# Kernel optimization log

Hardware: AMD Instinct MI355X
Metric: run time of the kernel (lower is better)

Reference implementation:

```python
import jax, jax.numpy as jnp
import numpy as np

B, T, C = 2, 2048, 1024
N_HEAD, N_GROUP = 16, 4
N_KV = N_HEAD // N_GROUP          # 4
HEAD_DIM = C // N_HEAD            # 64
ROPE_BASE = 10000.0
INIT_STD = 0.02


def setup_inputs() -> dict:
    key = jax.random.key(0)
    ks = jax.random.split(key, 5)
    kvC = N_KV * HEAD_DIM
    return {
        "x": jax.random.normal(ks[0], (B, T, C), jnp.float32),
        "w_q": jax.random.normal(ks[1], (C, C), jnp.float32) * INIT_STD,
        "b_q": jnp.zeros((C,), jnp.float32),
        "w_k": jax.random.normal(ks[2], (C, kvC), jnp.float32) * INIT_STD,
        "b_k": jnp.zeros((kvC,), jnp.float32),
        "w_v": jax.random.normal(ks[3], (C, kvC), jnp.float32) * INIT_STD,
        "b_v": jnp.zeros((kvC,), jnp.float32),
        "w_o": jax.random.normal(ks[4], (C, C), jnp.float32) * INIT_STD,
        "b_o": jnp.zeros((C,), jnp.float32),
    }


def reference(x, w_q, b_q, w_k, b_k, w_v, b_v, w_o, b_o):
    Bx, Tx, Cx = x.shape
    # projections (torch Linear math with weights stored as [in, out])
    q = (x @ w_q + b_q).reshape(Bx, Tx, N_HEAD, HEAD_DIM).transpose(0, 2, 1, 3)  # [B,H,T,hd]
    k = (x @ w_k + b_k).reshape(Bx, Tx, N_KV, HEAD_DIM).transpose(0, 2, 1, 3)    # [B,KV,T,hd]
    v = (x @ w_v + b_v).reshape(Bx, Tx, N_KV, HEAD_DIM).transpose(0, 2, 1, 3)

    # RoPE with INTERLEAVED pair convention: pairs are (dim 2i, dim 2i+1)
    inv_freq = 1.0 / (ROPE_BASE ** (jnp.arange(0, HEAD_DIM, 2, dtype=jnp.float32) / HEAD_DIM))
    freqs = jnp.arange(Tx, dtype=jnp.float32)[:, None] * inv_freq[None, :]       # [T, hd/2]
    cos, sin = jnp.cos(freqs), jnp.sin(freqs)

    def rope(t):
        tp = t.reshape(*t.shape[:-1], HEAD_DIM // 2, 2)
        e, o = tp[..., 0], tp[..., 1]          # even/odd lanes, [B,h,T,hd/2]
        er = e * cos - o * sin
        orr = e * sin + o * cos
        return jnp.stack([er, orr], axis=-1).reshape(t.shape)

    q, k = rope(q), rope(k)

    # GQA: duplicate each KV head n_group times (consecutively, like repeat_interleave)
    k = jnp.repeat(k, N_GROUP, axis=1)   # [B,H,T,hd]
    v = jnp.repeat(v, N_GROUP, axis=1)

    attn = jnp.einsum('bhqd,bhkd->bhqk', q, k) / np.sqrt(HEAD_DIM).astype(np.float32)
    causal = jnp.tril(jnp.ones((Tx, Tx), bool))
    attn = jnp.where(causal, attn, -jnp.inf)
    attn = jax.nn.softmax(attn, axis=-1)

    out = jnp.einsum('bhqk,bhkd->bhqd', attn, v)            # [B,H,T,hd]
    out = out.transpose(0, 2, 1, 3).reshape(Bx, Tx, Cx)
    return out @ w_o + b_o
```

## Files before the change

### kernel.cpp

```cpp
#include <hip/hip_runtime.h>
#include <hip/hip_bf16.h>

typedef __hip_bfloat16 bf16;
typedef __attribute__((ext_vector_type(8))) short short8_t;
typedef __attribute__((ext_vector_type(4))) short short4_t;
typedef __attribute__((ext_vector_type(4))) float f32x4;

#define B_SZ   2
#define T_SEQ  2048
#define C_DIM  1024
#define NH     16
#define NKV    4
#define HD     64
#define QKVW   1536
#define MTOK   (B_SZ * T_SEQ)

#define LOG2_BASE_OVER_32 0.4152410118609203f
#define Q_SCALE 0.1803368801111204f

__device__ __forceinline__ short f2bs(float f) {
    unsigned u = __float_as_uint(f);
    u += 0x7FFFu + ((u >> 16) & 1u);
    return (short)(u >> 16);
}
__device__ __forceinline__ short f2bs_trunc(float f) {
    return (short)(__float_as_uint(f) >> 16);
}
__device__ __forceinline__ float bs2f(short s) {
    unsigned u = ((unsigned)(unsigned short)s) << 16;
    return __uint_as_float(u);
}
__device__ __forceinline__ float dpp_xor1(float x) {
    return __int_as_float(
        __builtin_amdgcn_update_dpp(0, __float_as_int(x), 0xB1, 0xF, 0xF, true));
}

__device__ __forceinline__ void transpose_tile(
    const float* __restrict__ W, short* __restrict__ Wt,
    int K, int N, int n0, int k0, int tid)
{
    __shared__ float tile[32][33];
    int tx = tid & 31, ty = tid >> 5;
    #pragma unroll
    for (int i = 0; i < 4; ++i)
        tile[ty + 8 * i][tx] = W[(size_t)(k0 + ty + 8 * i) * N + n0 + tx];
    __syncthreads();
    #pragma unroll
    for (int i = 0; i < 4; ++i)
        Wt[(size_t)(n0 + ty + 8 * i) * K + k0 + tx] = f2bs(tile[tx][ty + 8 * i]);
}

__global__ __launch_bounds__(256) void prep_kernel(
    const float* __restrict__ x,
    const float* __restrict__ w_q, const float* __restrict__ w_k,
    const float* __restrict__ w_v, const float* __restrict__ w_o,
    const float* __restrict__ b_q, const float* __restrict__ b_k,
    const float* __restrict__ b_v,
    short* __restrict__ Xb, short* __restrict__ Wqkv, short* __restrict__ Wto,
    float* __restrict__ Bqkv, float2* __restrict__ Tab)
{
    int blk = blockIdx.x, tid = threadIdx.x;
    if (blk < 4096) {
        int i = blk * 1024 + tid * 4;
        float4 v = *(const float4*)(x + i);
        short4_t o;
        o[0] = f2bs(v.x); o[1] = f2bs(v.y); o[2] = f2bs(v.z); o[3] = f2bs(v.w);
        *(short4_t*)(Xb + i) = o;
    } else if (blk < 5120) {
        int l = blk - 4096;
        transpose_tile(w_q, Wqkv, C_DIM, C_DIM, (l & 31) * 32, (l >> 5) * 32, tid);
    } else if (blk < 5376) {
        int l = blk - 5120;
        transpose_tile(w_k, Wqkv + (size_t)1024 * C_DIM, C_DIM, 256,
                       (l & 7) * 32, (l >> 3) * 32, tid);
    } else if (blk < 5632) {
        int l = blk - 5376;
        transpose_tile(w_v, Wqkv + (size_t)1280 * C_DIM, C_DIM, 256,
                       (l & 7) * 32, (l >> 3) * 32, tid);
    } else if (blk < 6656) {
        int l = blk - 5632;
        transpose_tile(w_o, Wto, C_DIM, C_DIM, (l & 31) * 32, (l >> 5) * 32, tid);
    } else if (blk < 6662) {
        int i = (blk - 6656) * 256 + tid;
        float v;
        if (i < 1024)      v = b_q[i];
        else if (i < 1280) v = b_k[i - 1024];
        else               v = b_v[i - 1280];
        Bqkv[i] = v;
    } else {
        int idx = (blk - 6662) * 256 + tid;
        int t = idx >> 5, i = idx & 31;
        float ang = (float)t * exp2f(-(float)i * LOG2_BASE_OVER_32);
        Tab[idx] = make_float2(cosf(ang), sinf(ang));
    }
}

__global__ __launch_bounds__(256) void gemm_qkv(
    const short* __restrict__ A, const short* __restrict__ Bt,
    const float* __restrict__ bias, const float2* __restrict__ Tab,
    short* __restrict__ QKVb, short* __restrict__ Vt)
{
    __shared__ __align__(16) short smem[15360];
    short (*sA)[128][40] = (short(*)[128][40])smem;
    short (*sB)[64][40]  = (short(*)[64][40])(smem + 10240);

    const int K = C_DIM;
    int m0 = blockIdx.y * 128;
    int n0 = blockIdx.x * 64;
    int tid  = threadIdx.x;
    int w    = tid >> 6, lane = tid & 63;
    int quad = lane >> 4, l16 = lane & 15;
    int wm = w & 1, wn = w >> 1;

    f32x4 acc[4][2] = {};

    short8_t ra[2], rb;
    #pragma unroll
    for (int it = 0; it < 2; ++it) {
        int slot = tid + 256 * it, row = slot >> 2, g = (slot & 3) * 8;
        ra[it] = *(const short8_t*)(A + (size_t)(m0 + row) * K + g);
    }
    {
        int row = tid >> 2, g = (tid & 3) * 8;
        rb = *(const short8_t*)(Bt + (size_t)(n0 + row) * K + g);
    }

    int buf = 0;
    for (int k0 = 0; k0 < K; k0 += 32, buf ^= 1) {
        #pragma unroll
        for (int it = 0; it < 2; ++it) {
            int slot = tid + 256 * it, row = slot >> 2, g = (slot & 3) * 8;
            *(short8_t*)&sA[buf][row][g] = ra[it];
        }
        {
            int row = tid >> 2, g = (tid & 3) * 8;
            *(short8_t*)&sB[buf][row][g] = rb;
        }
        if (k0 + 32 < K) {
            #pragma unroll
            for (int it = 0; it < 2; ++it) {
                int slot = tid + 256 * it, row = slot >> 2, g = (slot & 3) * 8;
                ra[it] = *(const short8_t*)(A + (size_t)(m0 + row) * K + k0 + 32 + g);
            }
            int row = tid >> 2, g = (tid & 3) * 8;
            rb = *(const short8_t*)(Bt + (size_t)(n0 + row) * K + k0 + 32 + g);
        }
        __syncthreads();

        short8_t af[4], bfr[2];
        #pragma unroll
        for (int mt = 0; mt < 4; ++mt)
            af[mt] = *(const short8_t*)&sA[buf][wm * 64 + mt * 16 + l16][quad * 8];
        #pragma unroll
        for (int nt = 0; nt < 2; ++nt)
            bfr[nt] = *(const short8_t*)&sB[buf][wn * 32 + nt * 16 + l16][quad * 8];
        #pragma unroll
        for (int mt = 0; mt < 4; ++mt)
            #pragma unroll
            for (int nt = 0; nt < 2; ++nt)
                acc[mt][nt] = __builtin_amdgcn_mfma_f32_16x16x32_bf16(
                    af[mt], bfr[nt], acc[mt][nt], 0, 0, 0);
    }

    if (n0 < 1280) {
        float scale = (n0 < 1024) ? Q_SCALE : 1.0f;
        float sgn   = (l16 & 1) ? 1.0f : -1.0f;
        #pragma unroll
        for (int nt = 0; nt < 2; ++nt) {
            int col = n0 + wn * 32 + nt * 16 + l16;
            int ip  = (col & 63) >> 1;
            float bv = bias[col];
            #pragma unroll
            for (int mt = 0; mt < 4; ++mt) {
                #pragma unroll
                for (int r = 0; r < 4; ++r) {
                    int row = m0 + wm * 64 + mt * 16 + quad * 4 + r;
                    float v = acc[mt][nt][r] + bv;
                    float po = dpp_xor1(v);
                    float2 cs = Tab[(row & (T_SEQ - 1)) * 32 + ip];
                    float res = (v * cs.x + sgn * po * cs.y) * scale;
                    QKVb[(size_t)row * QKVW + col] = f2bs(res);
                }
            }
        }
    } else {
        __syncthreads();
        short (*sT)[136] = (short(*)[136])smem;
        #pragma unroll
        for (int nt = 0; nt < 2; ++nt) {
            int col_l = wn * 32 + nt * 16 + l16;
            float bv = bias[n0 + col_l];
            #pragma unroll
            for (int mt = 0; mt < 4; ++mt)
                #pragma unroll
                for (int r = 0; r < 4; ++r)
                    sT[col_l][wm * 64 + mt * 16 + quad * 4 + r] =
                        f2bs(acc[mt][nt][r] + bv);
        }
        __syncthreads();
        int d0 = n0 - 1280;
        #pragma unroll
        for (int it = 0; it < 4; ++it) {
            int slot = tid + 256 * it;
            int dl = slot >> 4, seg = (slot & 15) * 8;
            *(short8_t*)(Vt + (size_t)(d0 + dl) * MTOK + m0 + seg) =
                *(const short8_t*)&sT[dl][seg];
        }
    }
}

__global__ __launch_bounds__(256) void gemm_mfma_o(
    const short* __restrict__ A, const short* __restrict__ Bt,
    const float* __restrict__ bias, float* __restrict__ C,
    int M, int N, int K)
{
    __shared__ __align__(16) short smem[15360];
    short (*sA)[128][40] = (short(*)[128][40])smem;
    short (*sB)[64][40]  = (short(*)[64][40])(smem + 10240);

    int m0 = blockIdx.y * 128;
    int n0 = blockIdx.x * 64;
    int tid  = threadIdx.x;
    int w    = tid >> 6, lane = tid & 63;
    int quad = lane >> 4, l16 = lane & 15;
    int wm = w & 1, wn = w >> 1;

    f32x4 acc[4][2] = {};

    short8_t ra[2], rb;
    #pragma unroll
    for (int it = 0; it < 2; ++it) {
        int slot = tid + 256 * it, row = slot >> 2, g = (slot & 3) * 8;
        ra[it] = *(const short8_t*)(A + (size_t)(m0 + row) * K + g);
    }
    {
        int row = tid >> 2, g = (tid & 3) * 8;
        rb = *(const short8_t*)(Bt + (size_t)(n0 + row) * K + g);
    }

    int buf = 0;
    for (int k0 = 0; k0 < K; k0 += 32, buf ^= 1) {
        #pragma unroll
        for (int it = 0; it < 2; ++it) {
            int slot = tid + 256 * it, row = slot >> 2, g = (slot & 3) * 8;
            *(short8_t*)&sA[buf][row][g] = ra[it];
        }
        {
            int row = tid >> 2, g = (tid & 3) * 8;
            *(short8_t*)&sB[buf][row][g] = rb;
        }
        if (k0 + 32 < K) {
            #pragma unroll
            for (int it = 0; it < 2; ++it) {
                int slot = tid + 256 * it, row = slot >> 2, g = (slot & 3) * 8;
                ra[it] = *(const short8_t*)(A + (size_t)(m0 + row) * K + k0 + 32 + g);
            }
            int row = tid >> 2, g = (tid & 3) * 8;
            rb = *(const short8_t*)(Bt + (size_t)(n0 + row) * K + k0 + 32 + g);
        }
        __syncthreads();

        short8_t af[4], bfr[2];
        #pragma unroll
        for (int mt = 0; mt < 4; ++mt)
            af[mt] = *(const short8_t*)&sA[buf][wm * 64 + mt * 16 + l16][quad * 8];
        #pragma unroll
        for (int nt = 0; nt < 2; ++nt)
            bfr[nt] = *(const short8_t*)&sB[buf][wn * 32 + nt * 16 + l16][quad * 8];
        #pragma unroll
        for (int mt = 0; mt < 4; ++mt)
            #pragma unroll
            for (int nt = 0; nt < 2; ++nt)
                acc[mt][nt] = __builtin_amdgcn_mfma_f32_16x16x32_bf16(
                    af[mt], bfr[nt], acc[mt][nt], 0, 0, 0);
    }

    #pragma unroll
    for (int mt = 0; mt < 4; ++mt) {
        #pragma unroll
        for (int nt = 0; nt < 2; ++nt) {
            int col = n0 + wn * 32 + nt * 16 + l16;
            float bv = bias[col];
            #pragma unroll
            for (int r = 0; r < 4; ++r) {
                int row = m0 + wm * 64 + mt * 16 + quad * 4 + r;
                C[(size_t)row * N + col] = acc[mt][nt][r] + bv;
            }
        }
    }
}

__global__ __launch_bounds__(256) void attn_mfma9(
    const short* __restrict__ QKV, const short* __restrict__ Vt,
    short* __restrict__ O)
{
    __shared__ __align__(16) short sK [64][72];
    __shared__ __align__(16) short sVt[64][72];
    __shared__ __align__(16) short sP [4][16][72];

    const int tid  = threadIdx.x;
    const int w    = tid >> 6;
    const int lane = tid & 63;
    const int quad = lane >> 4;
    const int l16  = lane & 15;

    int blk = blockIdx.x;
    int grp = blk & 7;
    int tq  = 127 - (blk >> 3);
    int kvh = grp & 3;
    int b   = grp >> 2;
    int h   = kvh * 4 + w;
    int ct  = tq >> 2;
    int tg  = tq * 16 + l16;

    const short* qptr = QKV + ((size_t)(b * T_SEQ) + tq * 16 + l16) * QKVW + h * HD;
    short8_t qf0 = *(const short8_t*)(qptr + quad * 8);
    short8_t qf1 = *(const short8_t*)(qptr + quad * 8 + 32);

    const short* kbase  = QKV + (size_t)b * T_SEQ * QKVW + 1024 + kvh * HD;
    const short* vtbase = Vt + (size_t)(kvh * HD) * MTOK + b * T_SEQ;

    float m_l = -INFINITY, l_l = 0.f;
    f32x4 oacc[4];
    #pragma unroll
    for (int dt = 0; dt < 4; ++dt) oacc[dt] = (f32x4){0.f, 0.f, 0.f, 0.f};

    const int kkey = tid >> 3, kd = (tid & 7) * 8;
    const int vdim = tid >> 3, vseg = (tid & 7) * 8;

    short8_t kr[2], vr[2];
    #pragma unroll
    for (int it = 0; it < 2; ++it) {
        kr[it] = *(const short8_t*)(kbase + (size_t)(kkey + 32 * it) * QKVW + kd);
        vr[it] = *(const short8_t*)(vtbase + (size_t)(vdim + 32 * it) * MTOK + vseg);
    }

    for (int c = 0; c <= ct; ++c) {
        __syncthreads();
        #pragma unroll
        for (int it = 0; it < 2; ++it) {
            *(short8_t*)&sK [kkey + 32 * it][kd]   = kr[it];
            *(short8_t*)&sVt[vdim + 32 * it][vseg] = vr[it];
        }
        __syncthreads();
        if (c < ct) {
            int jn = (c + 1) * 64;
            #pragma unroll
            for (int it = 0; it < 2; ++it) {
                kr[it] = *(const short8_t*)(kbase + (size_t)(jn + kkey + 32 * it) * QKVW + kd);
                vr[it] = *(const short8_t*)(vtbase + (size_t)(vdim + 32 * it) * MTOK + jn + vseg);
            }
        }

        f32x4 sacc[4];
        #pragma unroll
        for (int kt = 0; kt < 4; ++kt) {
            f32x4 z = {0.f, 0.f, 0.f, 0.f};
            short8_t kf0 = *(const short8_t*)&sK[l16 + 16 * kt][quad * 8];
            short8_t kf1 = *(const short8_t*)&sK[l16 + 16 * kt][quad * 8 + 32];
            z = __builtin_amdgcn_mfma_f32_16x16x32_bf16(kf0, qf0, z, 0, 0, 0);
            z = __builtin_amdgcn_mfma_f32_16x16x32_bf16(kf1, qf1, z, 0, 0, 0);
            sacc[kt] = z;
        }

        if (c == ct) {
            int j0 = c * 64;
            #pragma unroll
            for (int kt = 0; kt < 4; ++kt)
                #pragma unroll
                for (int r = 0; r < 4; ++r)
                    if (j0 + 16 * kt + quad * 4 + r > tg) sacc[kt][r] = -INFINITY;
        }

        float vmax = sacc[0][0];
        #pragma unroll
        for (int kt = 0; kt < 4; ++kt)
            #pragma unroll
            for (int r = 0; r < 4; ++r) vmax = fmaxf(vmax, sacc[kt][r]);
        vmax = fmaxf(vmax, __shfl_xor(vmax, 16));
        vmax = fmaxf(vmax, __shfl_xor(vmax, 32));
        float mnew = fmaxf(m_l, vmax);
        float al = exp2f(m_l - mnew);
        m_l = mnew;

        float psum = 0.f;
        #pragma unroll
        for (int kt = 0; kt < 4; ++kt) {
            short4_t pk;
            #pragma unroll
            for (int r = 0; r < 4; ++r) {
                float p = exp2f(sacc[kt][r] - mnew);
                psum += p;
                pk[r] = f2bs_trunc(p);
            }
            *(short4_t*)&sP[w][l16][16 * kt + 4 * quad] = pk;
        }
        psum += __shfl_xor(psum, 16);
        psum += __shfl_xor(psum, 32);
        l_l = l_l * al + psum;

        if (__any(al < 1.f)) {
            #pragma unroll
            for (int r = 0; r < 4; ++r) {
                float alr = __shfl(al, quad * 4 + r);
                #pragma unroll
                for (int dt = 0; dt < 4; ++dt) oacc[dt][r] *= alr;
            }
        }

        short8_t pf0 = *(const short8_t*)&sP[w][l16][quad * 8];
        short8_t pf1 = *(const short8_t*)&sP[w][l16][quad * 8 + 32];
        #pragma unroll
        for (int dt = 0; dt < 4; ++dt) {
            short8_t vf0 = *(const short8_t*)&sVt[16 * dt + l16][quad * 8];
            short8_t vf1 = *(const short8_t*)&sVt[16 * dt + l16][quad * 8 + 32];
            oacc[dt] = __builtin_amdgcn_mfma_f32_16x16x32_bf16(pf0, vf0, oacc[dt], 0, 0, 0);
            oacc[dt] = __builtin_amdgcn_mfma_f32_16x16x32_bf16(pf1, vf1, oacc[dt], 0, 0, 0);
        }
    }

    #pragma unroll
    for (int r = 0; r < 4; ++r) {
        int m = quad * 4 + r;
        float lr = __shfl(l_l, quad * 4 + r);
        float inv = __builtin_amdgcn_rcpf(lr);
        #pragma unroll
        for (int dt = 0; dt < 4; ++dt)
            O[((size_t)b * T_SEQ + tq * 16 + m) * C_DIM + h * HD + 16 * dt + l16] =
                f2bs(oacc[dt][r] * inv);
    }
}

extern "C" void kernel_launch(void* const* d_in, const int* in_sizes, int n_in,
                              void* d_out, int out_size, void* d_ws, size_t ws_size,
                              hipStream_t stream)
{
    const float* x   = (const float*)d_in[0];
    const float* w_q = (const float*)d_in[1];
    const float* b_q = (const float*)d_in[2];
    const float* w_k = (const float*)d_in[3];
    const float* b_k = (const float*)d_in[4];
    const float* w_v = (const float*)d_in[5];
    const float* b_v = (const float*)d_in[6];
    const float* w_o = (const float*)d_in[7];
    const float* b_o = (const float*)d_in[8];
    float* out = (float*)d_out;

    char* ws = (char*)d_ws;
    short*  Xb   = (short*) (ws);
    short*  Ab   = (short*) (ws + ((size_t)8  << 20));
    short*  QKVb = (short*) (ws + ((size_t)16 << 20));
    short*  Wqkv = (short*) (ws + ((size_t)28 << 20));
    short*  Wto  = (short*) (ws + ((size_t)31 << 20));
    float*  Bqkv = (float*) (ws + ((size_t)33 << 20));
    float2* Tab  = (float2*)(ws + ((size_t)33 << 20) + 8192);
    short*  Vt   = (short*) (ws + ((size_t)34 << 20));

    const int M = MTOK;

    prep_kernel<<<6918, 256, 0, stream>>>(
        x, w_q, w_k, w_v, w_o, b_q, b_k, b_v, Xb, Wqkv, Wto, Bqkv, Tab);

    gemm_qkv<<<dim3(QKVW / 64, M / 128), 256, 0, stream>>>(
        Xb, Wqkv, Bqkv, Tab, QKVb, Vt);

    attn_mfma9<<<B_SZ * NKV * 128, 256, 0, stream>>>(QKVb, Vt, Ab);

    gemm_mfma_o<<<dim3(C_DIM / 64, M / 128), 256, 0, stream>>>(
        Ab, Wto, b_o, out, M, C_DIM, C_DIM);
}
```

Before: 174.9 us.

## Pair causal query tiles per attention block and deepen GEMM K-step to 64

The attention kernel now gives each block two query tiles, p and 127-p, so every block does about the same causal work and each K/V tile loaded into shared memory serves both tiles. The grid is halved to match. Separately, both GEMM kernels stage 64-wide K slices instead of 32, halving the number of loop iterations and barriers. The cost is more shared memory and more registers per thread, which may lower occupancy, and each attention block now carries two sets of accumulators.

```diff
diff --git a/kernel.cpp b/kernel.cpp
--- a/kernel.cpp
+++ b/kernel.cpp
@@ -100,9 +100,9 @@
     const float* __restrict__ bias, const float2* __restrict__ Tab,
     short* __restrict__ QKVb, short* __restrict__ Vt)
 {
-    __shared__ __align__(16) short smem[15360];
-    short (*sA)[128][40] = (short(*)[128][40])smem;
-    short (*sB)[64][40]  = (short(*)[64][40])(smem + 10240);
+    __shared__ __align__(16) short smem[26112];
+    short (*sA)[128][68] = (short(*)[128][68])smem;
+    short (*sB)[64][68]  = (short(*)[64][68])(smem + 17408);
 
     const int K = C_DIM;
     int m0 = blockIdx.y * 128;
@@ -114,52 +114,60 @@
 
     f32x4 acc[4][2] = {};
 
-    short8_t ra[2], rb;
+    short8_t ra[4], rb[2];
+    #pragma unroll
+    for (int it = 0; it < 4; ++it) {
+        int slot = tid + 256 * it, row = slot >> 3, g = (slot & 7) * 8;
+        ra[it] = *(const short8_t*)(A + (size_t)(m0 + row) * K + g);
+    }
     #pragma unroll
     for (int it = 0; it < 2; ++it) {
-        int slot = tid + 256 * it, row = slot >> 2, g = (slot & 3) * 8;
-        ra[it] = *(const short8_t*)(A + (size_t)(m0 + row) * K + g);
-    }
-    {
-        int row = tid >> 2, g = (tid & 3) * 8;
-        rb = *(const short8_t*)(Bt + (size_t)(n0 + row) * K + g);
+        int slot = tid + 256 * it, row = slot >> 3, g = (slot & 7) * 8;
+        rb[it] = *(const short8_t*)(Bt + (size_t)(n0 + row) * K + g);
     }
 
     int buf = 0;
-    for (int k0 = 0; k0 < K; k0 += 32, buf ^= 1) {
+    for (int k0 = 0; k0 < K; k0 += 64, buf ^= 1) {
+        #pragma unroll
+        for (int it = 0; it < 4; ++it) {
+            int slot = tid + 256 * it, row = slot >> 3, g = (slot & 7) * 8;
+            *(short8_t*)&sA[buf][row][g] = ra[it];
+        }
         #pragma unroll
         for (int it = 0; it < 2; ++it) {
-            int slot = tid + 256 * it, row = slot >> 2, g = (slot & 3) * 8;
-            *(short8_t*)&sA[buf][row][g] = ra[it];
-        }
-        {
-            int row = tid >> 2, g = (tid & 3) * 8;
-            *(short8_t*)&sB[buf][row][g] = rb;
-        }
-        if (k0 + 32 < K) {
+            int slot = tid + 256 * it, row = slot >> 3, g = (slot & 7) * 8;
+            *(short8_t*)&sB[buf][row][g] = rb[it];
+        }
+        if (k0 + 64 < K) {
+            #pragma unroll
+            for (int it = 0; it < 4; ++it) {
+                int slot = tid + 256 * it, row = slot >> 3, g = (slot & 7) * 8;
+                ra[it] = *(const short8_t*)(A + (size_t)(m0 + row) * K + k0 + 64 + g);
+            }
             #pragma unroll
             for (int it = 0; it < 2; ++it) {
-                int slot = tid + 256 * it, row = slot >> 2, g = (slot & 3) * 8;
-                ra[it] = *(const short8_t*)(A + (size_t)(m0 + row) * K + k0 + 32 + g);
-            }
-            int row = tid >> 2, g = (tid & 3) * 8;
-            rb = *(const short8_t*)(Bt + (size_t)(n0 + row) * K + k0 + 32 + g);
+                int slot = tid + 256 * it, row = slot >> 3, g = (slot & 7) * 8;
+                rb[it] = *(const short8_t*)(Bt + (size_t)(n0 + row) * K + k0 + 64 + g);
+            }
         }
         __syncthreads();
 
-        short8_t af[4], bfr[2];
-        #pragma unroll
-        for (int mt = 0; mt < 4; ++mt)
-            af[mt] = *(const short8_t*)&sA[buf][wm * 64 + mt * 16 + l16][quad * 8];
-        #pragma unroll
-        for (int nt = 0; nt < 2; ++nt)
-            bfr[nt] = *(const short8_t*)&sB[buf][wn * 32 + nt * 16 + l16][quad * 8];
-        #pragma unroll
-        for (int mt = 0; mt < 4; ++mt)
+        #pragma unroll
+        for (int h = 0; h < 2; ++h) {
+            short8_t af[4], bfr[2];
+            #pragma unroll
+            for (int mt = 0; mt < 4; ++mt)
+                af[mt] = *(const short8_t*)&sA[buf][wm * 64 + mt * 16 + l16][quad * 8 + 32 * h];
             #pragma unroll
             for (int nt = 0; nt < 2; ++nt)
-                acc[mt][nt] = __builtin_amdgcn_mfma_f32_16x16x32_bf16(
-                    af[mt], bfr[nt], acc[mt][nt], 0, 0, 0);
+                bfr[nt] = *(const short8_t*)&sB[buf][wn * 32 + nt * 16 + l16][quad * 8 + 32 * h];
+            #pragma unroll
+            for (int mt = 0; mt < 4; ++mt)
+                #pragma unroll
+                for (int nt = 0; nt < 2; ++nt)
+                    acc[mt][nt] = __builtin_amdgcn_mfma_f32_16x16x32_bf16(
+                        af[mt], bfr[nt], acc[mt][nt], 0, 0, 0);
+        }
     }
 
     if (n0 < 1280) {
@@ -214,9 +222,9 @@
     const float* __restrict__ bias, float* __restrict__ C,
     int M, int N, int K)
 {
-    __shared__ __align__(16) short smem[15360];
-    short (*sA)[128][40] = (short(*)[128][40])smem;
-    short (*sB)[64][40]  = (short(*)[64][40])(smem + 10240);
+    __shared__ __align__(16) short smem[26112];
+    short (*sA)[128][68] = (short(*)[128][68])smem;
+    short (*sB)[64][68]  = (short(*)[64][68])(smem + 17408);
 
     int m0 = blockIdx.y * 128;
     int n0 = blockIdx.x * 64;
@@ -227,52 +235,60 @@
 
     f32x4 acc[4][2] = {};
 
-    short8_t ra[2], rb;
+    short8_t ra[4], rb[2];
+    #pragma unroll
+    for (int it = 0; it < 4; ++it) {
+        int slot = tid + 256 * it, row = slot >> 3, g = (slot & 7) * 8;
+        ra[it] = *(const short8_t*)(A + (size_t)(m0 + row) * K + g);
+    }
     #pragma unroll
     for (int it = 0; it < 2; ++it) {
-        int slot = tid + 256 * it, row = slot >> 2, g = (slot & 3) * 8;
-        ra[it] = *(const short8_t*)(A + (size_t)(m0 + row) * K + g);
-    }
-    {
-        int row = tid >> 2, g = (tid & 3) * 8;
-        rb = *(const short8_t*)(Bt + (size_t)(n0 + row) * K + g);
+        int slot = tid + 256 * it, row = slot >> 3, g = (slot & 7) * 8;
+        rb[it] = *(const short8_t*)(Bt + (size_t)(n0 + row) * K + g);
     }
 
     int buf = 0;
-    for (int k0 = 0; k0 < K; k0 += 32, buf ^= 1) {
+    for (int k0 = 0; k0 < K; k0 += 64, buf ^= 1) {
+        #pragma unroll
+        for (int it = 0; it < 4; ++it) {
+            int slot = tid + 256 * it, row = slot >> 3, g = (slot & 7) * 8;
+            *(short8_t*)&sA[buf][row][g] = ra[it];
+        }
         #pragma unroll
         for (int it = 0; it < 2; ++it) {
-            int slot = tid + 256 * it, row = slot >> 2, g = (slot & 3) * 8;
-            *(short8_t*)&sA[buf][row][g] = ra[it];
-        }
-        {
-            int row = tid >> 2, g = (tid & 3) * 8;
-            *(short8_t*)&sB[buf][row][g] = rb;
-        }
-        if (k0 + 32 < K) {
+            int slot = tid + 256 * it, row = slot >> 3, g = (slot & 7) * 8;
+            *(short8_t*)&sB[buf][row][g] = rb[it];
+        }
+        if (k0 + 64 < K) {
+            #pragma unroll
+            for (int it = 0; it < 4; ++it) {
+                int slot = tid + 256 * it, row = slot >> 3, g = (slot & 7) * 8;
+                ra[it] = *(const short8_t*)(A + (size_t)(m0 + row) * K + k0 + 64 + g);
+            }
             #pragma unroll
             for (int it = 0; it < 2; ++it) {
-                int slot = tid + 256 * it, row = slot >> 2, g = (slot & 3) * 8;
-                ra[it] = *(const short8_t*)(A + (size_t)(m0 + row) * K + k0 + 32 + g);
-            }
-            int row = tid >> 2, g = (tid & 3) * 8;
-            rb = *(const short8_t*)(Bt + (size_t)(n0 + row) * K + k0 + 32 + g);
+                int slot = tid + 256 * it, row = slot >> 3, g = (slot & 7) * 8;
+                rb[it] = *(const short8_t*)(Bt + (size_t)(n0 + row) * K + k0 + 64 + g);
+            }
         }
         __syncthreads();
 
-        short8_t af[4], bfr[2];
-        #pragma unroll
-        for (int mt = 0; mt < 4; ++mt)
-            af[mt] = *(const short8_t*)&sA[buf][wm * 64 + mt * 16 + l16][quad * 8];
-        #pragma unroll
-        for (int nt = 0; nt < 2; ++nt)
-            bfr[nt] = *(const short8_t*)&sB[buf][wn * 32 + nt * 16 + l16][quad * 8];
-        #pragma unroll
-        for (int mt = 0; mt < 4; ++mt)
+        #pragma unroll
+        for (int h = 0; h < 2; ++h) {
+            short8_t af[4], bfr[2];
+            #pragma unroll
+            for (int mt = 0; mt < 4; ++mt)
+                af[mt] = *(const short8_t*)&sA[buf][wm * 64 + mt * 16 + l16][quad * 8 + 32 * h];
             #pragma unroll
             for (int nt = 0; nt < 2; ++nt)
-                acc[mt][nt] = __builtin_amdgcn_mfma_f32_16x16x32_bf16(
-                    af[mt], bfr[nt], acc[mt][nt], 0, 0, 0);
+                bfr[nt] = *(const short8_t*)&sB[buf][wn * 32 + nt * 16 + l16][quad * 8 + 32 * h];
+            #pragma unroll
+            for (int mt = 0; mt < 4; ++mt)
+                #pragma unroll
+                for (int nt = 0; nt < 2; ++nt)
+                    acc[mt][nt] = __builtin_amdgcn_mfma_f32_16x16x32_bf16(
+                        af[mt], bfr[nt], acc[mt][nt], 0, 0, 0);
+        }
     }
 
     #pragma unroll
@@ -290,13 +306,13 @@
     }
 }
 
-__global__ __launch_bounds__(256) void attn_mfma9(
+__global__ __launch_bounds__(256) void attn_mfma10(
     const short* __restrict__ QKV, const short* __restrict__ Vt,
     short* __restrict__ O)
 {
     __shared__ __align__(16) short sK [64][72];
     __shared__ __align__(16) short sVt[64][72];
-    __shared__ __align__(16) short sP [4][16][72];
+    __shared__ __align__(16) short sP [4][2][16][72];
 
     const int tid  = threadIdx.x;
     const int w    = tid >> 6;
@@ -306,24 +322,31 @@
 
     int blk = blockIdx.x;
     int grp = blk & 7;
-    int tq  = 127 - (blk >> 3);
+    int p   = blk >> 3;
     int kvh = grp & 3;
     int b   = grp >> 2;
     int h   = kvh * 4 + w;
-    int ct  = tq >> 2;
-    int tg  = tq * 16 + l16;
-
-    const short* qptr = QKV + ((size_t)(b * T_SEQ) + tq * 16 + l16) * QKVW + h * HD;
-    short8_t qf0 = *(const short8_t*)(qptr + quad * 8);
-    short8_t qf1 = *(const short8_t*)(qptr + quad * 8 + 32);
+    int tqA = p, tqB = 127 - p;
+    int ctA = tqA >> 2, ctB = tqB >> 2;
+    int tgA = tqA * 16 + l16, tgB = tqB * 16 + l16;
+
+    const short* qpA = QKV + ((size_t)(b * T_SEQ) + tgA) * QKVW + h * HD;
+    short8_t qA0 = *(const short8_t*)(qpA + quad * 8);
+    short8_t qA1 = *(const short8_t*)(qpA + quad * 8 + 32);
+    const short* qpB = QKV + ((size_t)(b * T_SEQ) + tgB) * QKVW + h * HD;
+    short8_t qB0 = *(const short8_t*)(qpB + quad * 8);
+    short8_t qB1 = *(const short8_t*)(qpB + quad * 8 + 32);
 
     const short* kbase  = QKV + (size_t)b * T_SEQ * QKVW + 1024 + kvh * HD;
     const short* vtbase = Vt + (size_t)(kvh * HD) * MTOK + b * T_SEQ;
 
-    float m_l = -INFINITY, l_l = 0.f;
-    f32x4 oacc[4];
-    #pragma unroll
-    for (int dt = 0; dt < 4; ++dt) oacc[dt] = (f32x4){0.f, 0.f, 0.f, 0.f};
+    float mA = -INFINITY, lA = 0.f, mB = -INFINITY, lB = 0.f;
+    f32x4 oA[4], oB[4];
+    #pragma unroll
+    for (int dt = 0; dt < 4; ++dt) {
+        oA[dt] = (f32x4){0.f, 0.f, 0.f, 0.f};
+        oB[dt] = (f32x4){0.f, 0.f, 0.f, 0.f};
+    }
 
     const int kkey = tid >> 3, kd = (tid & 7) * 8;
     const int vdim = tid >> 3, vseg = (tid & 7) * 8;
@@ -335,7 +358,7 @@
         vr[it] = *(const short8_t*)(vtbase + (size_t)(vdim + 32 * it) * MTOK + vseg);
     }
 
-    for (int c = 0; c <= ct; ++c) {
+    for (int c = 0; c <= ctB; ++c) {
         __syncthreads();
         #pragma unroll
         for (int it = 0; it < 2; ++it) {
@@ -343,7 +366,7 @@
             *(short8_t*)&sVt[vdim + 32 * it][vseg] = vr[it];
         }
         __syncthreads();
-        if (c < ct) {
+        if (c < ctB) {
             int jn = (c + 1) * 64;
             #pragma unroll
             for (int it = 0; it < 2; ++it) {
@@ -352,82 +375,149 @@
             }
         }
 
-        f32x4 sacc[4];
+        bool actA = (c <= ctA);
+
+        f32x4 sa[4], sb[4];
         #pragma unroll
         for (int kt = 0; kt < 4; ++kt) {
-            f32x4 z = {0.f, 0.f, 0.f, 0.f};
             short8_t kf0 = *(const short8_t*)&sK[l16 + 16 * kt][quad * 8];
             short8_t kf1 = *(const short8_t*)&sK[l16 + 16 * kt][quad * 8 + 32];
-            z = __builtin_amdgcn_mfma_f32_16x16x32_bf16(kf0, qf0, z, 0, 0, 0);
-            z = __builtin_amdgcn_mfma_f32_16x16x32_bf16(kf1, qf1, z, 0, 0, 0);
-            sacc[kt] = z;
-        }
-
-        if (c == ct) {
-            int j0 = c * 64;
+            f32x4 zb = {0.f, 0.f, 0.f, 0.f};
+            zb = __builtin_amdgcn_mfma_f32_16x16x32_bf16(kf0, qB0, zb, 0, 0, 0);
+            zb = __builtin_amdgcn_mfma_f32_16x16x32_bf16(kf1, qB1, zb, 0, 0, 0);
+            sb[kt] = zb;
+            if (actA) {
+                f32x4 za = {0.f, 0.f, 0.f, 0.f};
+                za = __builtin_amdgcn_mfma_f32_16x16x32_bf16(kf0, qA0, za, 0, 0, 0);
+                za = __builtin_amdgcn_mfma_f32_16x16x32_bf16(kf1, qA1, za, 0, 0, 0);
+                sa[kt] = za;
+            }
+        }
+
+        int j0 = c * 64;
+        if (c == ctB) {
             #pragma unroll
             for (int kt = 0; kt < 4; ++kt)
                 #pragma unroll
                 for (int r = 0; r < 4; ++r)
-                    if (j0 + 16 * kt + quad * 4 + r > tg) sacc[kt][r] = -INFINITY;
-        }
-
-        float vmax = sacc[0][0];
-        #pragma unroll
-        for (int kt = 0; kt < 4; ++kt)
-            #pragma unroll
-            for (int r = 0; r < 4; ++r) vmax = fmaxf(vmax, sacc[kt][r]);
-        vmax = fmaxf(vmax, __shfl_xor(vmax, 16));
-        vmax = fmaxf(vmax, __shfl_xor(vmax, 32));
-        float mnew = fmaxf(m_l, vmax);
-        float al = exp2f(m_l - mnew);
-        m_l = mnew;
-
-        float psum = 0.f;
-        #pragma unroll
-        for (int kt = 0; kt < 4; ++kt) {
-            short4_t pk;
+                    if (j0 + 16 * kt + quad * 4 + r > tgB) sb[kt][r] = -INFINITY;
+        }
+        if (actA && c == ctA) {
+            #pragma unroll
+            for (int kt = 0; kt < 4; ++kt)
+                #pragma unroll
+                for (int r = 0; r < 4; ++r)
+                    if (j0 + 16 * kt + quad * 4 + r > tgA) sa[kt][r] = -INFINITY;
+        }
+
+        float alB;
+        {
+            float vmax = sb[0][0];
+            #pragma unroll
+            for (int kt = 0; kt < 4; ++kt)
+                #pragma unroll
+                for (int r = 0; r < 4; ++r) vmax = fmaxf(vmax, sb[kt][r]);
+            vmax = fmaxf(vmax, __shfl_xor(vmax, 16));
+            vmax = fmaxf(vmax, __shfl_xor(vmax, 32));
+            float mnew = fmaxf(mB, vmax);
+            alB = exp2f(mB - mnew);
+            mB = mnew;
+            float psum = 0.f;
+            #pragma unroll
+            for (int kt = 0; kt < 4; ++kt) {
+                short4_t pk;
+                #pragma unroll
+                for (int r = 0; r < 4; ++r) {
+                    float pv = exp2f(sb[kt][r] - mnew);
+                    psum += pv;
+                    pk[r] = f2bs_trunc(pv);
+                }
+                *(short4_t*)&sP[w][1][l16][16 * kt + 4 * quad] = pk;
+            }
+            psum += __shfl_xor(psum, 16);
+            psum += __shfl_xor(psum, 32);
+            lB = lB * alB + psum;
+        }
+        float alA = 1.f;
+        if (actA) {
+            float vmax = sa[0][0];
+            #pragma unroll
+            for (int kt = 0; kt < 4; ++kt)
+                #pragma unroll
+                for (int r = 0; r < 4; ++r) vmax = fmaxf(vmax, sa[kt][r]);
+            vmax = fmaxf(vmax, __shfl_xor(vmax, 16));
+            vmax = fmaxf(vmax, __shfl_xor(vmax, 32));
+            float mnew = fmaxf(mA, vmax);
+            alA = exp2f(mA - mnew);
+            mA = mnew;
+            float psum = 0.f;
+            #pragma unroll
+            for (int kt = 0; kt < 4; ++kt) {
+                short4_t pk;
+                #pragma unroll
+                for (int r = 0; r < 4; ++r) {
+                    float pv = exp2f(sa[kt][r] - mnew);
+                    psum += pv;
+                    pk[r] = f2bs_trunc(pv);
+                }
+                *(short4_t*)&sP[w][0][l16][16 * kt + 4 * quad] = pk;
+            }
+            psum += __shfl_xor(psum, 16);
+            psum += __shfl_xor(psum, 32);
+            lA = lA * alA + psum;
+        }
+
+        if (__any(alB < 1.f)) {
             #pragma unroll
             for (int r = 0; r < 4; ++r) {
-                float p = exp2f(sacc[kt][r] - mnew);
-                psum += p;
-                pk[r] = f2bs_trunc(p);
-            }
-            *(short4_t*)&sP[w][l16][16 * kt + 4 * quad] = pk;
-        }
-        psum += __shfl_xor(psum, 16);
-        psum += __shfl_xor(psum, 32);
-        l_l = l_l * al + psum;
-
-        if (__any(al < 1.f)) {
+                float ar = __shfl(alB, quad * 4 + r);
+                #pragma unroll
+                for (int dt = 0; dt < 4; ++dt) oB[dt][r] *= ar;
+            }
+        }
+        if (actA && __any(alA < 1.f)) {
             #pragma unroll
             for (int r = 0; r < 4; ++r) {
-                float alr = __shfl(al, quad * 4 + r);
-                #pragma unroll
-                for (int dt = 0; dt < 4; ++dt) oacc[dt][r] *= alr;
-            }
-        }
-
-        short8_t pf0 = *(const short8_t*)&sP[w][l16][quad * 8];
-        short8_t pf1 = *(const short8_t*)&sP[w][l16][quad * 8 + 32];
+                float ar = __shfl(alA, quad * 4 + r);
+                #pragma unroll
+                for (int dt = 0; dt < 4; ++dt) oA[dt][r] *= ar;
+            }
+        }
+
+        short8_t pB0 = *(const short8_t*)&sP[w][1][l16][quad * 8];
+        short8_t pB1 = *(const short8_t*)&sP[w][1][l16][quad * 8 + 32];
+        short8_t pA0, pA1;
+        if (actA) {
+            pA0 = *(const short8_t*)&sP[w][0][l16][quad * 8];
+            pA1 = *(const short8_t*)&sP[w][0][l16][quad * 8 + 32];
+        }
         #pragma unroll
         for (int dt = 0; dt < 4; ++dt) {
             short8_t vf0 = *(const short8_t*)&sVt[16 * dt + l16][quad * 8];
             short8_t vf1 = *(const short8_t*)&sVt[16 * dt + l16][quad * 8 + 32];
-            oacc[dt] = __builtin_amdgcn_mfma_f32_16x16x32_bf16(pf0, vf0, oacc[dt], 0, 0, 0);
-            oacc[dt] = __builtin_amdgcn_mfma_f32_16x16x32_bf16(pf1, vf1, oacc[dt], 0, 0, 0);
+            oB[dt] = __builtin_amdgcn_mfma_f32_16x16x32_bf16(pB0, vf0, oB[dt], 0, 0, 0);
+            oB[dt] = __builtin_amdgcn_mfma_f32_16x16x32_bf16(pB1, vf1, oB[dt], 0, 0, 0);
+            if (actA) {
+                oA[dt] = __builtin_amdgcn_mfma_f32_16x16x32_bf16(pA0, vf0, oA[dt], 0, 0, 0);
+                oA[dt] = __builtin_amdgcn_mfma_f32_16x16x32_bf16(pA1, vf1, oA[dt], 0, 0, 0);
+            }
         }
     }
 
     #pragma unroll
     for (int r = 0; r < 4; ++r) {
         int m = quad * 4 + r;
-        float lr = __shfl(l_l, quad * 4 + r);
-        float inv = __builtin_amdgcn_rcpf(lr);
-        #pragma unroll
-        for (int dt = 0; dt < 4; ++dt)
-            O[((size_t)b * T_SEQ + tq * 16 + m) * C_DIM + h * HD + 16 * dt + l16] =
-                f2bs(oacc[dt][r] * inv);
+        float lrA = __shfl(lA, quad * 4 + r);
+        float lrB = __shfl(lB, quad * 4 + r);
+        float invA = __builtin_amdgcn_rcpf(lrA);
+        float invB = __builtin_amdgcn_rcpf(lrB);
+        #pragma unroll
+        for (int dt = 0; dt < 4; ++dt) {
+            O[((size_t)b * T_SEQ + tqA * 16 + m) * C_DIM + h * HD + 16 * dt + l16] =
+                f2bs(oA[dt][r] * invA);
+            O[((size_t)b * T_SEQ + tqB * 16 + m) * C_DIM + h * HD + 16 * dt + l16] =
+                f2bs(oB[dt][r] * invB);
+        }
     }
 }
 
@@ -464,7 +554,7 @@
     gemm_qkv<<<dim3(QKVW / 64, M / 128), 256, 0, stream>>>(
         Xb, Wqkv, Bqkv, Tab, QKVb, Vt);
 
-    attn_mfma9<<<B_SZ * NKV * 128, 256, 0, stream>>>(QKVb, Vt, Ab);
+    attn_mfma10<<<B_SZ * NKV * 64, 256, 0, stream>>>(QKVb, Vt, Ab);
 
     gemm_mfma_o<<<dim3(C_DIM / 64, M / 128), 256, 0, stream>>>(
         Ab, Wto, b_o, out, M, C_DIM, C_DIM);
```

Result: slower. 282.6 us (+61.5%).

## Split attention KV loop across two blocks and add combine kernel

Applied to the files above, without the earlier changes.

Splits each query tile's causal KV loop into two interleaved halves (even and odd 64-key chunks), run by separate blocks, which doubles the grid to 2048 blocks. Each half writes its unnormalized partial output plus its running max and sum, and a new combine kernel merges them with log-sum-exp rescaling. The goal is more parallelism and less tail imbalance from the triangular causal work. The cost is an extra kernel launch, extra global traffic for the partials, and an extra bf16 rounding of the unnormalized partial outputs.

```diff
diff --git a/kernel.cpp b/kernel.cpp
--- a/kernel.cpp
+++ b/kernel.cpp
@@ -290,9 +290,10 @@
     }
 }
 
-__global__ __launch_bounds__(256) void attn_mfma9(
+__global__ __launch_bounds__(256) void attn_mfma11(
     const short* __restrict__ QKV, const short* __restrict__ Vt,
-    short* __restrict__ O)
+    short* __restrict__ Op0, short* __restrict__ Op1,
+    float* __restrict__ Mp, float* __restrict__ Lp)
 {
     __shared__ __align__(16) short sK [64][72];
     __shared__ __align__(16) short sVt[64][72];
@@ -306,14 +307,15 @@
 
     int blk = blockIdx.x;
     int grp = blk & 7;
-    int tq  = 127 - (blk >> 3);
+    int s   = (blk >> 3) & 1;
+    int tq  = 127 - (blk >> 4);
     int kvh = grp & 3;
     int b   = grp >> 2;
     int h   = kvh * 4 + w;
     int ct  = tq >> 2;
     int tg  = tq * 16 + l16;
 
-    const short* qptr = QKV + ((size_t)(b * T_SEQ) + tq * 16 + l16) * QKVW + h * HD;
+    const short* qptr = QKV + ((size_t)(b * T_SEQ) + tg) * QKVW + h * HD;
     short8_t qf0 = *(const short8_t*)(qptr + quad * 8);
     short8_t qf1 = *(const short8_t*)(qptr + quad * 8 + 32);
 
@@ -329,13 +331,16 @@
     const int vdim = tid >> 3, vseg = (tid & 7) * 8;
 
     short8_t kr[2], vr[2];
-    #pragma unroll
-    for (int it = 0; it < 2; ++it) {
-        kr[it] = *(const short8_t*)(kbase + (size_t)(kkey + 32 * it) * QKVW + kd);
-        vr[it] = *(const short8_t*)(vtbase + (size_t)(vdim + 32 * it) * MTOK + vseg);
-    }
-
-    for (int c = 0; c <= ct; ++c) {
+    {
+        int j0 = s * 64;
+        #pragma unroll
+        for (int it = 0; it < 2; ++it) {
+            kr[it] = *(const short8_t*)(kbase + (size_t)(j0 + kkey + 32 * it) * QKVW + kd);
+            vr[it] = *(const short8_t*)(vtbase + (size_t)(vdim + 32 * it) * MTOK + j0 + vseg);
+        }
+    }
+
+    for (int c = s; c <= ct; c += 2) {
         __syncthreads();
         #pragma unroll
         for (int it = 0; it < 2; ++it) {
@@ -343,8 +348,8 @@
             *(short8_t*)&sVt[vdim + 32 * it][vseg] = vr[it];
         }
         __syncthreads();
-        if (c < ct) {
-            int jn = (c + 1) * 64;
+        if (c + 2 <= ct) {
+            int jn = (c + 2) * 64;
             #pragma unroll
             for (int it = 0; it < 2; ++it) {
                 kr[it] = *(const short8_t*)(kbase + (size_t)(jn + kkey + 32 * it) * QKVW + kd);
@@ -419,16 +424,46 @@
         }
     }
 
+    int tix = (b * NH + h) * 128 + tq;
+    if (quad == 0) {
+        Mp[(size_t)(s * 4096 + tix) * 16 + l16] = m_l;
+        Lp[(size_t)(s * 4096 + tix) * 16 + l16] = l_l;
+    }
+    short* Op = s ? Op1 : Op0;
     #pragma unroll
     for (int r = 0; r < 4; ++r) {
-        int m = quad * 4 + r;
-        float lr = __shfl(l_l, quad * 4 + r);
-        float inv = __builtin_amdgcn_rcpf(lr);
+        int q = quad * 4 + r;
         #pragma unroll
         for (int dt = 0; dt < 4; ++dt)
-            O[((size_t)b * T_SEQ + tq * 16 + m) * C_DIM + h * HD + 16 * dt + l16] =
-                f2bs(oacc[dt][r] * inv);
-    }
+            Op[(size_t)tix * 1024 + q * 64 + 16 * dt + l16] = f2bs(oacc[dt][r]);
+    }
+}
+
+__global__ __launch_bounds__(256) void attn_combine(
+    const short* __restrict__ Op0, const short* __restrict__ Op1,
+    const float* __restrict__ Mp, const float* __restrict__ Lp,
+    short* __restrict__ Ab)
+{
+    int blk = blockIdx.x;
+    int tid = threadIdx.x;
+    int q = tid >> 4, d0 = (tid & 15) * 4;
+    int tq = blk & 127, bh = blk >> 7, h = bh & 15, b = bh >> 4;
+
+    float m0 = Mp[(size_t)blk * 16 + q];
+    float m1 = Mp[(size_t)(4096 + blk) * 16 + q];
+    float l0 = Lp[(size_t)blk * 16 + q];
+    float l1 = Lp[(size_t)(4096 + blk) * 16 + q];
+    float ms = fmaxf(m0, m1);
+    float a0 = exp2f(m0 - ms), a1 = exp2f(m1 - ms);
+    float inv = __builtin_amdgcn_rcpf(l0 * a0 + l1 * a1);
+
+    short4_t o0 = *(const short4_t*)&Op0[(size_t)blk * 1024 + q * 64 + d0];
+    short4_t o1 = *(const short4_t*)&Op1[(size_t)blk * 1024 + q * 64 + d0];
+    short4_t res;
+    #pragma unroll
+    for (int i = 0; i < 4; ++i)
+        res[i] = f2bs((bs2f(o0[i]) * a0 + bs2f(o1[i]) * a1) * inv);
+    *(short4_t*)&Ab[((size_t)(b * T_SEQ + tq * 16 + q)) * C_DIM + h * HD + d0] = res;
 }
 
 extern "C" void kernel_launch(void* const* d_in, const int* in_sizes, int n_in,
@@ -455,6 +490,10 @@
     float*  Bqkv = (float*) (ws + ((size_t)33 << 20));
     float2* Tab  = (float2*)(ws + ((size_t)33 << 20) + 8192);
     short*  Vt   = (short*) (ws + ((size_t)34 << 20));
+    short*  Op0  = Xb;
+    short*  Op1  = (short*) (ws + ((size_t)36 << 20));
+    float*  Mp   = (float*) (ws + ((size_t)44 << 20));
+    float*  Lp   = (float*) (ws + ((size_t)44 << 20) + (1 << 19));
 
     const int M = MTOK;
 
@@ -464,7 +503,9 @@
     gemm_qkv<<<dim3(QKVW / 64, M / 128), 256, 0, stream>>>(
         Xb, Wqkv, Bqkv, Tab, QKVb, Vt);
 
-    attn_mfma9<<<B_SZ * NKV * 128, 256, 0, stream>>>(QKVb, Vt, Ab);
+    attn_mfma11<<<2048, 256, 0, stream>>>(QKVb, Vt, Op0, Op1, Mp, Lp);
+
+    attn_combine<<<4096, 256, 0, stream>>>(Op0, Op1, Mp, Lp, Ab);
 
     gemm_mfma_o<<<dim3(C_DIM / 64, M / 128), 256, 0, stream>>>(
         Ab, Wto, b_o, out, M, C_DIM, C_DIM);
```

After: 179.3 us. 2.5% more time.
